# Kernel tuning notes

Measured on AMD Instinct MI355X. Metric: run time of the kernel, lower is better.

The kernel has to match this reference:

```python
import jax, jax.numpy as jnp
import numpy as np

N, H, K = 50000, 32, 15
C_IN, C_OUT = 64, 128
KP_EXTENT = 1.0
BN_EPS = 1e-5
SLOPE = 0.2


def setup_inputs() -> dict:
    key = jax.random.key(0)
    k1, k2, k3, k4, k5 = jax.random.split(key, 5)
    points = jax.random.normal(k1, (N, 3), dtype=jnp.float32)
    x = jax.random.normal(k2, (N, C_IN), dtype=jnp.float32)
    neighbors = jax.random.randint(k3, (N, H), 0, N, dtype=jnp.int32)
    # kernel points: fixed disposition inside the kernel sphere
    kernel_points = jax.random.normal(k4, (K, 3), dtype=jnp.float32) * (0.5 * KP_EXTENT)
    weights = jax.random.normal(k5, (K, C_IN, C_OUT), dtype=jnp.float32) / np.sqrt(K * C_IN)
    gamma = jnp.ones((C_OUT,), dtype=jnp.float32)
    beta = jnp.zeros((C_OUT,), dtype=jnp.float32)
    return {"points": points, "x": x, "neighbors": neighbors,
            "kernel_points": kernel_points, "weights": weights,
            "gamma": gamma, "beta": beta}


def reference(points, x, neighbors, kernel_points, weights, gamma, beta):
    # --- KPConv: irregular neighbor gather + kernel-point weighted sum ---
    # relative neighbor positions: [N, H, 3]
    neighb_pos = points[neighbors] - points[:, None, :]
    # squared distances to each kernel point: [N, H, K]
    sq_dist = jnp.sum((neighb_pos[:, :, None, :] - kernel_points[None, None, :, :]) ** 2, axis=-1)
    # linear correlation (influence), clipped at 0: [N, H, K]
    influence = jnp.maximum(0.0, 1.0 - jnp.sqrt(sq_dist) / KP_EXTENT)
    # gathered neighbor features: [N, H, C_in]
    neighb_x = x[neighbors]
    # per-kernel-point aggregated features: [N, K, C_in]
    weighted_feat = jnp.einsum('nhk,nhc->nkc', influence, neighb_x)
    # apply per-kernel-point weight matrices and sum: [N, C_out]
    out = jnp.einsum('nkc,kcd->nd', weighted_feat, weights)
    # --- BatchNorm1d (training-mode batch statistics) ---
    mean = jnp.mean(out, axis=0)
    var = jnp.var(out, axis=0)
    y = (out - mean) * jax.lax.rsqrt(var + BN_EPS) * gamma + beta
    # --- LeakyReLU(0.2) ---
    return jnp.where(y > 0, y, SLOPE * y)
```

## Files before the change

kernel.cpp:

```cpp
#include <hip/hip_runtime.h>
#include <hip/hip_bf16.h>

#define N_PTS 50000
#define H_NB 32
#define K_KP 15
#define C_IN 64
#define C_OUT 128
#define KC 960
#define M_PAD 50048
#define M_TILE 32
#define PPW 8
#define WFS 968
#define XG_SUB 68
#define XG_PLANE 552
#define XG_WAVE (4*XG_PLANE)
#define BN_EPS 1e-5f
#define SLOPE 0.2f

typedef __attribute__((ext_vector_type(8))) __bf16 bf16x8;
typedef __attribute__((ext_vector_type(8))) unsigned short ushort8;
typedef __attribute__((ext_vector_type(4))) float f32x4;

__device__ __forceinline__ unsigned short bfbits(float f){
  return __builtin_bit_cast(unsigned short, (__bf16)f);
}
__device__ __forceinline__ bf16x8 ld_bf8(const unsigned short* p){
  return __builtin_bit_cast(bf16x8, *(const uint4*)p);
}
__device__ __forceinline__ void gload16(const void* g, void* l){
  __builtin_amdgcn_global_load_lds(
      (__attribute__((address_space(1))) void*)(g),
      (__attribute__((address_space(3))) void*)(l), 16, 0, 0);
}

__global__ __launch_bounds__(256) void xprep_kernel(const float* __restrict__ x,
                                                    unsigned short* __restrict__ xbf){
  int t = blockIdx.x*blockDim.x + threadIdx.x;
  if (t < N_PTS*C_IN/8) {
    float4 a = ((const float4*)x)[2*t], b = ((const float4*)x)[2*t+1];
    ushort8 o;
    o[0]=bfbits(a.x); o[1]=bfbits(a.y); o[2]=bfbits(a.z); o[3]=bfbits(a.w);
    o[4]=bfbits(b.x); o[5]=bfbits(b.y); o[6]=bfbits(b.z); o[7]=bfbits(b.w);
    *(ushort8*)(xbf + 8*t) = o;
  }
}

__global__ __launch_bounds__(256) void prep_kernel(const float* __restrict__ W,
                                                   unsigned short* __restrict__ Wt,
                                                   float* __restrict__ stats){
  __shared__ float tile[32][33];
  if (blockIdx.x == 0 && blockIdx.y == 0 && threadIdx.x < 2*C_OUT)
    stats[threadIdx.x] = 0.f;
  const int kc0 = blockIdx.x * 32, d0 = blockIdx.y * 32;
  const int r = threadIdx.x >> 5, c = threadIdx.x & 31;
  #pragma unroll
  for (int rr = 0; rr < 4; ++rr) {
    int row = rr*8 + r;
    tile[row][c] = W[(size_t)(kc0+row)*C_OUT + d0 + c];
  }
  __syncthreads();
  #pragma unroll
  for (int rr = 0; rr < 4; ++rr) {
    int dr = rr*8 + r;
    Wt[(size_t)(d0+dr)*KC + kc0 + c] = bfbits(tile[c][dr]);
  }
}

template<bool SPLIT>
__global__ __launch_bounds__(256, SPLIT ? 4 : 2) void kpconv_core(
    const float* __restrict__ points,
    const float* __restrict__ x,
    const unsigned short* __restrict__ xbf,
    const int*   __restrict__ neighbors,
    const float* __restrict__ kpts,
    const unsigned short* __restrict__ Wt,
    unsigned short* __restrict__ wfg,
    float* __restrict__ out_pre,
    float* __restrict__ stats)
{
  __shared__ __align__(16) unsigned short xg[4 * XG_WAVE];
  __shared__ unsigned short wf_lds[SPLIT ? 8 : M_TILE*WFS];
  __shared__ float sh_sum[SPLIT ? 1 : C_OUT];
  __shared__ float sh_sq [SPLIT ? 1 : C_OUT];

  const int tid  = threadIdx.x;
  const int w    = tid >> 6;
  const int lane = tid & 63;
  const int l15  = lane & 15;
  const int lq   = lane >> 4;
  const int base = blockIdx.x * M_TILE;

  float kqx, kqy, kqz;
  if (l15 < K_KP) { kqx = kpts[l15*3+0]; kqy = kpts[l15*3+1]; kqz = kpts[l15*3+2]; }
  else            { kqx = 1e3f; kqy = 0.f; kqz = 0.f; }

  unsigned short* xgw = &xg[w * XG_WAVE];

  if constexpr (SPLIT) {
    int   idx_c, idx_n = 0, idx_nn = 0;
    float pcx, pcy, pcz, pnx = 0, pny = 0, pnz = 0;
    float ccx, ccy, ccz, cnx = 0, cny = 0, cnz = 0, c2x = 0, c2y = 0, c2z = 0;
    uint2 xr[8];
    {
      int n0 = base + w*PPW;  int nc0 = n0 < N_PTS ? n0 : N_PTS-1;
      idx_c = neighbors[nc0*H_NB + (lane & 31)];
      ccx = points[nc0*3+0]; ccy = points[nc0*3+1]; ccz = points[nc0*3+2];
      const float* pp = points + (size_t)idx_c*3;
      pcx = pp[0]; pcy = pp[1]; pcz = pp[2];
      #pragma unroll
      for (int it = 0; it < 8; ++it) {
        int nh = __shfl(idx_c, 4*it + lq);
        xr[it] = *(const uint2*)&xbf[(size_t)nh*C_IN + 4*l15];
      }
      int n1 = n0 + 1;  int nc1 = n1 < N_PTS ? n1 : N_PTS-1;
      idx_n = neighbors[nc1*H_NB + (lane & 31)];
      cnx = points[nc1*3+0]; cny = points[nc1*3+1]; cnz = points[nc1*3+2];
      const float* pq = points + (size_t)idx_n*3;
      pnx = pq[0]; pny = pq[1]; pnz = pq[2];
    }

    #pragma unroll 1
    for (int p = 0; p < PPW; ++p) {
      float rx = pcx - ccx, ry = pcy - ccy, rz = pcz - ccz;
      bf16x8 afrag;
      #pragma unroll
      for (int j = 0; j < 8; ++j) {
        int h = (lq << 3) + j;
        float dx = __shfl(rx, h) - kqx;
        float dy = __shfl(ry, h) - kqy;
        float dz = __shfl(rz, h) - kqz;
        float f  = 1.f - sqrtf(dx*dx + dy*dy + dz*dz);
        afrag[j] = (__bf16)(f > 0.f ? f : 0.f);
      }

      #pragma unroll
      for (int it = 0; it < 8; ++it) {
        int ei = XG_PLANE*(l15 >> 2) + XG_SUB*it + 16*lq + 4*(l15 & 3);
        *(uint2*)(xgw + ei) = xr[it];
      }

      if (p + 1 < PPW) {
        #pragma unroll
        for (int it = 0; it < 8; ++it) {
          int nh = __shfl(idx_n, 4*it + lq);
          xr[it] = *(const uint2*)&xbf[(size_t)nh*C_IN + 4*l15];
        }
      }
      if (p + 2 < PPW) {
        int n2 = base + w*PPW + p + 2;  int nc2 = n2 < N_PTS ? n2 : N_PTS-1;
        idx_nn = neighbors[nc2*H_NB + (lane & 31)];
        c2x = points[nc2*3+0]; c2y = points[nc2*3+1]; c2z = points[nc2*3+2];
      }

      asm volatile("s_waitcnt lgkmcnt(0)" ::: "memory");

      ushort8 bbr[4];
      #pragma unroll
      for (int ct = 0; ct < 4; ++ct) {
        #pragma unroll
        for (int j = 0; j < 8; ++j)
          bbr[ct][j] = xgw[XG_PLANE*ct + XG_SUB*(2*lq + (j>>2)) + 16*(j&3) + l15];
      }

      f32x4 acc[4] = {{0,0,0,0},{0,0,0,0},{0,0,0,0},{0,0,0,0}};
      #pragma unroll
      for (int ct = 0; ct < 4; ++ct)
        acc[ct] = __builtin_amdgcn_mfma_f32_16x16x32_bf16(
            afrag, __builtin_bit_cast(bf16x8, bbr[ct]), acc[ct], 0, 0, 0);

      const int n_out = base + w*PPW + p;
      #pragma unroll
      for (int ct = 0; ct < 4; ++ct) {
        #pragma unroll
        for (int r = 0; r < 4; ++r) {
          int k = 4*lq + r;
          if (k < K_KP)
            xgw[72*k + ct*16 + l15] = bfbits(acc[ct][r]);
        }
      }
      asm volatile("s_waitcnt lgkmcnt(0)" ::: "memory");
      if (n_out < N_PTS) {
        uint4 c0 = *(const uint4*)(xgw + 72*(lane>>3) + 8*(lane&7));
        *(uint4*)(wfg + (size_t)n_out*KC + lane*8) = c0;
        if (lane < 56) {
          int ch = 64 + lane;
          uint4 c1 = *(const uint4*)(xgw + 72*(ch>>3) + 8*(ch&7));
          *(uint4*)(wfg + (size_t)n_out*KC + ch*8) = c1;
        }
      }
      asm volatile("s_waitcnt lgkmcnt(0)" ::: "memory");

      if (p + 1 < PPW) {
        pcx = pnx; pcy = pny; pcz = pnz;
        ccx = cnx; ccy = cny; ccz = cnz;
        idx_c = idx_n; idx_n = idx_nn;
        cnx = c2x; cny = c2y; cnz = c2z;
        if (p + 2 < PPW) {
          const float* pq = points + (size_t)idx_n*3;
          pnx = pq[0]; pny = pq[1]; pnz = pq[2];
        }
      }
    }
  } else {
    {
      int   idx_c, idx_n = 0, idx_nn = 0;
      float pcx, pcy, pcz, pnx = 0, pny = 0, pnz = 0;
      float ccx, ccy, ccz, cnx = 0, cny = 0, cnz = 0, c2x = 0, c2y = 0, c2z = 0;
      float4 xr[8];
      {
        int n0 = base + w*PPW;  int nc0 = n0 < N_PTS ? n0 : N_PTS-1;
        idx_c = neighbors[nc0*H_NB + (lane & 31)];
        ccx = points[nc0*3+0]; ccy = points[nc0*3+1]; ccz = points[nc0*3+2];
        const float* pp = points + (size_t)idx_c*3;
        pcx = pp[0]; pcy = pp[1]; pcz = pp[2];
        #pragma unroll
        for (int it = 0; it < 8; ++it) {
          int nh = __shfl(idx_c, 4*it + lq);
          xr[it] = *(const float4*)&x[(size_t)nh*C_IN + 4*l15];
        }
        int n1 = n0 + 1;  int nc1 = n1 < N_PTS ? n1 : N_PTS-1;
        idx_n = neighbors[nc1*H_NB + (lane & 31)];
        cnx = points[nc1*3+0]; cny = points[nc1*3+1]; cnz = points[nc1*3+2];
        const float* pq = points + (size_t)idx_n*3;
        pnx = pq[0]; pny = pq[1]; pnz = pq[2];
      }

      #pragma unroll 1
      for (int p = 0; p < PPW; ++p) {
        const int mpt = w*PPW + p;
        float rx = pcx - ccx, ry = pcy - ccy, rz = pcz - ccz;
        bf16x8 afrag;
        #pragma unroll
        for (int j = 0; j < 8; ++j) {
          int h = (lq << 3) + j;
          float dx = __shfl(rx, h) - kqx;
          float dy = __shfl(ry, h) - kqy;
          float dz = __shfl(rz, h) - kqz;
          float f  = 1.f - sqrtf(dx*dx + dy*dy + dz*dz);
          afrag[j] = (__bf16)(f > 0.f ? f : 0.f);
        }
        #pragma unroll
        for (int it = 0; it < 8; ++it) {
          float4 v = xr[it];
          unsigned lo = ((unsigned)bfbits(v.y) << 16) | bfbits(v.x);
          unsigned hi = ((unsigned)bfbits(v.w) << 16) | bfbits(v.z);
          int ei = XG_PLANE*(l15 >> 2) + XG_SUB*it + 16*lq + 4*(l15 & 3);
          uint2 val; val.x = lo; val.y = hi;
          *(uint2*)(xgw + ei) = val;
        }
        if (p + 1 < PPW) {
          #pragma unroll
          for (int it = 0; it < 8; ++it) {
            int nh = __shfl(idx_n, 4*it + lq);
            xr[it] = *(const float4*)&x[(size_t)nh*C_IN + 4*l15];
          }
        }
        if (p + 2 < PPW) {
          int n2 = base + w*PPW + p + 2;  int nc2 = n2 < N_PTS ? n2 : N_PTS-1;
          idx_nn = neighbors[nc2*H_NB + (lane & 31)];
          c2x = points[nc2*3+0]; c2y = points[nc2*3+1]; c2z = points[nc2*3+2];
        }
        asm volatile("s_waitcnt lgkmcnt(0)" ::: "memory");
        ushort8 bbr[4];
        #pragma unroll
        for (int ct = 0; ct < 4; ++ct) {
          #pragma unroll
          for (int j = 0; j < 8; ++j)
            bbr[ct][j] = xgw[XG_PLANE*ct + XG_SUB*(2*lq + (j>>2)) + 16*(j&3) + l15];
        }
        f32x4 acc[4] = {{0,0,0,0},{0,0,0,0},{0,0,0,0},{0,0,0,0}};
        #pragma unroll
        for (int ct = 0; ct < 4; ++ct)
          acc[ct] = __builtin_amdgcn_mfma_f32_16x16x32_bf16(
              afrag, __builtin_bit_cast(bf16x8, bbr[ct]), acc[ct], 0, 0, 0);
        #pragma unroll
        for (int ct = 0; ct < 4; ++ct) {
          #pragma unroll
          for (int r = 0; r < 4; ++r) {
            int k = 4*lq + r;
            if (k < K_KP)
              wf_lds[mpt*WFS + k*C_IN + ((ct ^ lq)*16) + l15] = bfbits(acc[ct][r]);
          }
        }
        if (p + 1 < PPW) {
          pcx = pnx; pcy = pny; pcz = pnz;
          ccx = cnx; ccy = cny; ccz = cnz;
          idx_c = idx_n; idx_n = idx_nn;
          cnx = c2x; cny = c2y; cnz = c2z;
          if (p + 2 < PPW) {
            const float* pq = points + (size_t)idx_n*3;
            pnx = pq[0]; pny = pq[1]; pnz = pq[2];
          }
        }
      }
    }

    __syncthreads();
    const int wd = w;
    f32x4 b00{0,0,0,0}, b01{0,0,0,0}, b10{0,0,0,0}, b11{0,0,0,0};
    const unsigned short* arow0 = &wf_lds[l15*WFS];
    const unsigned short* arow1 = arow0 + 16*WFS;
    const unsigned short* wrow0 = Wt + (size_t)(wd*32 + l15)*KC + lq*8;
    const unsigned short* wrow1 = wrow0 + (size_t)16*KC;
    #pragma unroll 6
    for (int ks = 0; ks < KC/32; ++ks) {
      int aoff = (ks*32 + lq*8) ^ ((((ks >> 1) >> 2) & 3) << 4);
      bf16x8 a0 = ld_bf8(arow0 + aoff);
      bf16x8 a1 = ld_bf8(arow1 + aoff);
      bf16x8 w0 = ld_bf8(wrow0 + ks*32);
      bf16x8 w1 = ld_bf8(wrow1 + ks*32);
      b00 = __builtin_amdgcn_mfma_f32_16x16x32_bf16(a0, w0, b00, 0, 0, 0);
      b01 = __builtin_amdgcn_mfma_f32_16x16x32_bf16(a0, w1, b01, 0, 0, 0);
      b10 = __builtin_amdgcn_mfma_f32_16x16x32_bf16(a1, w0, b10, 0, 0, 0);
      b11 = __builtin_amdgcn_mfma_f32_16x16x32_bf16(a1, w1, b11, 0, 0, 0);
    }
    float s0 = 0.f, q0 = 0.f, s1 = 0.f, q1 = 0.f;
    const int dcol0 = wd*32 + l15;
    #pragma unroll
    for (int mi = 0; mi < 2; ++mi) {
      const f32x4 A0 = mi ? b10 : b00;
      const f32x4 A1 = mi ? b11 : b01;
      #pragma unroll
      for (int r = 0; r < 4; ++r) {
        int n = base + mi*16 + 4*lq + r;
        if (n < N_PTS) {
          float v0 = A0[r], v1 = A1[r];
          out_pre[(size_t)n*C_OUT + dcol0]      = v0;
          out_pre[(size_t)n*C_OUT + dcol0 + 16] = v1;
          s0 += v0; q0 += v0*v0;
          s1 += v1; q1 += v1*v1;
        }
      }
    }
    s0 += __shfl_xor(s0, 16); s0 += __shfl_xor(s0, 32);
    q0 += __shfl_xor(q0, 16); q0 += __shfl_xor(q0, 32);
    s1 += __shfl_xor(s1, 16); s1 += __shfl_xor(s1, 32);
    q1 += __shfl_xor(q1, 16); q1 += __shfl_xor(q1, 32);
    if (lane < 16) {
      sh_sum[wd*32 + lane]      = s0;
      sh_sum[wd*32 + 16 + lane] = s1;
      sh_sq [wd*32 + lane]      = q0;
      sh_sq [wd*32 + 16 + lane] = q1;
    }
    __syncthreads();
    if (tid < C_OUT) {
      atomicAdd(&stats[tid],         sh_sum[tid]);
      atomicAdd(&stats[C_OUT + tid], sh_sq[tid]);
    }
  }
}

__global__ __launch_bounds__(256, 2) void gemm_kernel(
    const unsigned short* __restrict__ wfg,
    const unsigned short* __restrict__ Wt,
    float* __restrict__ out_pre,
    float* __restrict__ stats)
{
  __shared__ __align__(16) unsigned short Abuf[3][64*64];
  __shared__ __align__(16) unsigned short Bbuf[3][128*64];
  __shared__ float sh_sum[2][C_OUT];
  __shared__ float sh_sq [2][C_OUT];

  const int tid  = threadIdx.x;
  const int w    = tid >> 6;
  const int lane = tid & 63;
  const int l15  = lane & 15;
  const int lq   = lane >> 4;
  const int wm   = w >> 1;
  const int wn   = w & 1;
  const int m0   = blockIdx.x * 64;

  const int r8 = lane >> 3;
  const int cs = (lane & 7) ^ r8;

  auto stage = [&](int b, int kt){
    const int k0 = kt * 64;
    #pragma unroll
    for (int q = 0; q < 2; ++q) {
      int row = w*16 + q*8;
      gload16(wfg + (size_t)(m0 + row + r8)*KC + k0 + cs*8, &Abuf[b][row*64]);
    }
    #pragma unroll
    for (int q = 0; q < 4; ++q) {
      int row = w*32 + q*8;
      gload16(Wt + (size_t)(row + r8)*KC + k0 + cs*8, &Bbuf[b][row*64]);
    }
  };

  stage(0, 0);
  stage(1, 1);

  f32x4 acc[2][4] = {};
  const int NT = KC / 64;
  for (int ks = 0; ks < NT; ++ks) {
    if (ks + 1 < NT) {
      asm volatile("s_waitcnt vmcnt(6)" ::: "memory");
    } else {
      asm volatile("s_waitcnt vmcnt(0)" ::: "memory");
    }
    __builtin_amdgcn_sched_barrier(0);
    __builtin_amdgcn_s_barrier();
    asm volatile("" ::: "memory");
    if (ks + 2 < NT) stage((ks + 2) % 3, ks + 2);

    const unsigned short* A = Abuf[ks % 3];
    const unsigned short* B = Bbuf[ks % 3];
    #pragma unroll
    for (int kk = 0; kk < 2; ++kk) {
      const int cA = kk*4 + lq;
      bf16x8 af[2], bfr[4];
      #pragma unroll
      for (int mf = 0; mf < 2; ++mf) {
        int r = wm*32 + mf*16 + l15;
        af[mf] = ld_bf8(A + r*64 + ((cA ^ (r & 7)) * 8));
      }
      #pragma unroll
      for (int nf = 0; nf < 4; ++nf) {
        int r = wn*64 + nf*16 + l15;
        bfr[nf] = ld_bf8(B + r*64 + ((cA ^ (r & 7)) * 8));
      }
      #pragma unroll
      for (int mf = 0; mf < 2; ++mf)
        #pragma unroll
        for (int nf = 0; nf < 4; ++nf)
          acc[mf][nf] = __builtin_amdgcn_mfma_f32_16x16x32_bf16(af[mf], bfr[nf], acc[mf][nf], 0, 0, 0);
    }
  }

  float ssum[4] = {0,0,0,0}, ssq[4] = {0,0,0,0};
  #pragma unroll
  for (int mf = 0; mf < 2; ++mf) {
    #pragma unroll
    for (int nf = 0; nf < 4; ++nf) {
      #pragma unroll
      for (int r = 0; r < 4; ++r) {
        int m = m0 + wm*32 + mf*16 + 4*lq + r;
        if (m < N_PTS) {
          float v = acc[mf][nf][r];
          out_pre[(size_t)m*C_OUT + wn*64 + nf*16 + l15] = v;
          ssum[nf] += v; ssq[nf] += v*v;
        }
      }
    }
  }
  #pragma unroll
  for (int nf = 0; nf < 4; ++nf) {
    ssum[nf] += __shfl_xor(ssum[nf], 16); ssum[nf] += __shfl_xor(ssum[nf], 32);
    ssq[nf]  += __shfl_xor(ssq[nf], 16);  ssq[nf]  += __shfl_xor(ssq[nf], 32);
  }
  if (lane < 16) {
    #pragma unroll
    for (int nf = 0; nf < 4; ++nf) {
      sh_sum[wm][wn*64 + nf*16 + lane] = ssum[nf];
      sh_sq [wm][wn*64 + nf*16 + lane] = ssq[nf];
    }
  }
  __syncthreads();
  if (tid < C_OUT) {
    atomicAdd(&stats[tid],         sh_sum[0][tid] + sh_sum[1][tid]);
    atomicAdd(&stats[C_OUT + tid], sh_sq[0][tid] + sh_sq[1][tid]);
  }
}

__global__ __launch_bounds__(256) void bn_lrelu_kernel(float* __restrict__ out,
                                                       const float* __restrict__ stats,
                                                       const float* __restrict__ gamma,
                                                       const float* __restrict__ beta){
  __shared__ float sc_s[C_OUT], sh_s[C_OUT];
  if (threadIdx.x < C_OUT) {
    int d = threadIdx.x;
    float mean = stats[d] * (1.f/N_PTS);
    float var  = stats[C_OUT+d] * (1.f/N_PTS) - mean*mean;
    var = var > 0.f ? var : 0.f;
    float inv = rsqrtf(var + BN_EPS);
    float sc  = inv * gamma[d];
    sc_s[d] = sc;
    sh_s[d] = beta[d] - mean * sc;
  }
  __syncthreads();
  const int total4 = N_PTS*C_OUT/4;
  const float4* scp = (const float4*)sc_s;
  const float4* shp = (const float4*)sh_s;
  float4* o4 = (float4*)out;
  for (int t = blockIdx.x*blockDim.x + threadIdx.x; t < total4; t += gridDim.x*blockDim.x) {
    int col4 = t & (C_OUT/4 - 1);
    float4 v = o4[t];
    float4 sc = scp[col4], sh = shp[col4];
    float y0 = v.x*sc.x + sh.x;
    float y1 = v.y*sc.y + sh.y;
    float y2 = v.z*sc.z + sh.z;
    float y3 = v.w*sc.w + sh.w;
    v.x = y0 > 0.f ? y0 : SLOPE*y0;
    v.y = y1 > 0.f ? y1 : SLOPE*y1;
    v.z = y2 > 0.f ? y2 : SLOPE*y2;
    v.w = y3 > 0.f ? y3 : SLOPE*y3;
    o4[t] = v;
  }
}

extern "C" void kernel_launch(void* const* d_in, const int* in_sizes, int n_in,
                              void* d_out, int out_size, void* d_ws, size_t ws_size,
                              hipStream_t stream) {
  const float* points    = (const float*)d_in[0];
  const float* x         = (const float*)d_in[1];
  const int*   neighbors = (const int*)d_in[2];
  const float* kpts      = (const float*)d_in[3];
  const float* weights   = (const float*)d_in[4];
  const float* gamma     = (const float*)d_in[5];
  const float* beta      = (const float*)d_in[6];
  float* out = (float*)d_out;
  float* ws  = (float*)d_ws;
  unsigned short* Wt  = (unsigned short*)((char*)d_ws + 2048);
  unsigned short* wfg = (unsigned short*)((char*)d_ws + 2048 + 245760);
  unsigned short* xbf = (unsigned short*)d_out;
  const size_t need = 2048u + 245760u + (size_t)M_PAD*KC*2u;
  const bool split = (ws_size >= need);

  hipLaunchKernelGGL(prep_kernel, dim3(KC/32, C_OUT/32), dim3(256), 0, stream,
                     weights, Wt, ws);
  const int nblocks = (N_PTS + M_TILE - 1) / M_TILE;
  if (split) {
    hipLaunchKernelGGL(xprep_kernel, dim3((N_PTS*C_IN/8 + 255)/256), dim3(256), 0, stream,
                       x, xbf);
    kpconv_core<true><<<dim3(nblocks), dim3(256), 0, stream>>>(
        points, x, xbf, neighbors, kpts, Wt, wfg, out, ws);
    gemm_kernel<<<dim3(M_PAD/64), dim3(256), 0, stream>>>(wfg, Wt, out, ws);
  } else {
    kpconv_core<false><<<dim3(nblocks), dim3(256), 0, stream>>>(
        points, x, xbf, neighbors, kpts, Wt, wfg, out, ws);
  }
  hipLaunchKernelGGL(bn_lrelu_kernel, dim3(2048), dim3(256), 0, stream, out, ws, gamma, beta);
}
```

Before: 120.2 us.

## Gather neighbor features directly into double-buffered LDS with swizzled layout

In the split KPConv path, neighbor bf16 feature rows are now loaded straight from global memory into LDS with a direct-to-LDS load helper, instead of being staged through registers and then written to LDS. Two per-wave LDS buffers alternate, so the gather for the next point overlaps the MFMA and output work for the current one, and explicit vmcnt waits control when data is ready. An XOR swizzle on column chunks is meant to avoid bank conflicts when reading the B operand. This raises LDS use per block and depends on vmcnt counting that other outstanding global operations can disturb.

```diff
diff --git a/kernel.cpp b/kernel.cpp
--- a/kernel.cpp
+++ b/kernel.cpp
@@ -78,7 +78,7 @@
     float* __restrict__ out_pre,
     float* __restrict__ stats)
 {
-  __shared__ __align__(16) unsigned short xg[4 * XG_WAVE];
+  __shared__ __align__(16) unsigned short xg[SPLIT ? 4*4096 : 4*XG_WAVE];
   __shared__ unsigned short wf_lds[SPLIT ? 8 : M_TILE*WFS];
   __shared__ float sh_sum[SPLIT ? 1 : C_OUT];
   __shared__ float sh_sq [SPLIT ? 1 : C_OUT];
@@ -94,30 +94,42 @@
   if (l15 < K_KP) { kqx = kpts[l15*3+0]; kqy = kpts[l15*3+1]; kqz = kpts[l15*3+2]; }
   else            { kqx = 1e3f; kqy = 0.f; kqz = 0.f; }
 
-  unsigned short* xgw = &xg[w * XG_WAVE];
-
   if constexpr (SPLIT) {
+    unsigned short* xb0 = &xg[w * 4096];
+    unsigned short* xb1 = xb0 + 2048;
+
+    const int r8 = lane >> 3;
+    const int pc = lane & 7;
+
+    auto dma_point = [&](unsigned short* buf, int idx){
+      #pragma unroll
+      for (int it = 0; it < 4; ++it) {
+        int nh = __shfl(idx, 8*it + r8);
+        const unsigned short* src = xbf + (size_t)nh*C_IN + ((pc ^ (2*it)) * 8);
+        gload16(src, buf + it*512);
+      }
+    };
+
     int   idx_c, idx_n = 0, idx_nn = 0;
     float pcx, pcy, pcz, pnx = 0, pny = 0, pnz = 0;
     float ccx, ccy, ccz, cnx = 0, cny = 0, cnz = 0, c2x = 0, c2y = 0, c2z = 0;
-    uint2 xr[8];
     {
       int n0 = base + w*PPW;  int nc0 = n0 < N_PTS ? n0 : N_PTS-1;
       idx_c = neighbors[nc0*H_NB + (lane & 31)];
       ccx = points[nc0*3+0]; ccy = points[nc0*3+1]; ccz = points[nc0*3+2];
       const float* pp = points + (size_t)idx_c*3;
       pcx = pp[0]; pcy = pp[1]; pcz = pp[2];
-      #pragma unroll
-      for (int it = 0; it < 8; ++it) {
-        int nh = __shfl(idx_c, 4*it + lq);
-        xr[it] = *(const uint2*)&xbf[(size_t)nh*C_IN + 4*l15];
-      }
       int n1 = n0 + 1;  int nc1 = n1 < N_PTS ? n1 : N_PTS-1;
       idx_n = neighbors[nc1*H_NB + (lane & 31)];
       cnx = points[nc1*3+0]; cny = points[nc1*3+1]; cnz = points[nc1*3+2];
       const float* pq = points + (size_t)idx_n*3;
       pnx = pq[0]; pny = pq[1]; pnz = pq[2];
-    }
+      dma_point(xb0, idx_c);
+      dma_point(xb1, idx_n);
+    }
+
+    unsigned short* cur = xb0;
+    unsigned short* nxt = xb1;
 
     #pragma unroll 1
     for (int p = 0; p < PPW; ++p) {
@@ -133,40 +145,27 @@
         afrag[j] = (__bf16)(f > 0.f ? f : 0.f);
       }
 
-      #pragma unroll
-      for (int it = 0; it < 8; ++it) {
-        int ei = XG_PLANE*(l15 >> 2) + XG_SUB*it + 16*lq + 4*(l15 & 3);
-        *(uint2*)(xgw + ei) = xr[it];
-      }
-
-      if (p + 1 < PPW) {
-        #pragma unroll
-        for (int it = 0; it < 8; ++it) {
-          int nh = __shfl(idx_n, 4*it + lq);
-          xr[it] = *(const uint2*)&xbf[(size_t)nh*C_IN + 4*l15];
-        }
-      }
       if (p + 2 < PPW) {
         int n2 = base + w*PPW + p + 2;  int nc2 = n2 < N_PTS ? n2 : N_PTS-1;
         idx_nn = neighbors[nc2*H_NB + (lane & 31)];
         c2x = points[nc2*3+0]; c2y = points[nc2*3+1]; c2z = points[nc2*3+2];
       }
 
-      asm volatile("s_waitcnt lgkmcnt(0)" ::: "memory");
-
-      ushort8 bbr[4];
+      if (p + 1 < PPW) { asm volatile("s_waitcnt vmcnt(4)" ::: "memory"); }
+      else             { asm volatile("s_waitcnt vmcnt(0)" ::: "memory"); }
+      __builtin_amdgcn_sched_barrier(0);
+
+      f32x4 acc[4] = {{0,0,0,0},{0,0,0,0},{0,0,0,0},{0,0,0,0}};
       #pragma unroll
       for (int ct = 0; ct < 4; ++ct) {
+        ushort8 b;
+        const int pcr = ((2*ct + (l15 >> 3)) ^ (2*lq)) * 8 + (l15 & 7);
         #pragma unroll
         for (int j = 0; j < 8; ++j)
-          bbr[ct][j] = xgw[XG_PLANE*ct + XG_SUB*(2*lq + (j>>2)) + 16*(j&3) + l15];
-      }
-
-      f32x4 acc[4] = {{0,0,0,0},{0,0,0,0},{0,0,0,0},{0,0,0,0}};
-      #pragma unroll
-      for (int ct = 0; ct < 4; ++ct)
+          b[j] = cur[lq*512 + j*64 + pcr];
         acc[ct] = __builtin_amdgcn_mfma_f32_16x16x32_bf16(
-            afrag, __builtin_bit_cast(bf16x8, bbr[ct]), acc[ct], 0, 0, 0);
+            afrag, __builtin_bit_cast(bf16x8, b), acc[ct], 0, 0, 0);
+      }
 
       const int n_out = base + w*PPW + p;
       #pragma unroll
@@ -175,16 +174,16 @@
         for (int r = 0; r < 4; ++r) {
           int k = 4*lq + r;
           if (k < K_KP)
-            xgw[72*k + ct*16 + l15] = bfbits(acc[ct][r]);
+            cur[72*k + ct*16 + l15] = bfbits(acc[ct][r]);
         }
       }
       asm volatile("s_waitcnt lgkmcnt(0)" ::: "memory");
       if (n_out < N_PTS) {
-        uint4 c0 = *(const uint4*)(xgw + 72*(lane>>3) + 8*(lane&7));
+        uint4 c0 = *(const uint4*)(cur + 72*(lane>>3) + 8*(lane&7));
         *(uint4*)(wfg + (size_t)n_out*KC + lane*8) = c0;
         if (lane < 56) {
           int ch = 64 + lane;
-          uint4 c1 = *(const uint4*)(xgw + 72*(ch>>3) + 8*(ch&7));
+          uint4 c1 = *(const uint4*)(cur + 72*(ch>>3) + 8*(ch&7));
           *(uint4*)(wfg + (size_t)n_out*KC + ch*8) = c1;
         }
       }
@@ -198,10 +197,13 @@
         if (p + 2 < PPW) {
           const float* pq = points + (size_t)idx_n*3;
           pnx = pq[0]; pny = pq[1]; pnz = pq[2];
-        }
+          dma_point(cur, idx_n);
+        }
+        unsigned short* t = cur; cur = nxt; nxt = t;
       }
     }
   } else {
+    unsigned short* xgw = &xg[w * XG_WAVE];
     {
       int   idx_c, idx_n = 0, idx_nn = 0;
       float pcx, pcy, pcz, pnx = 0, pny = 0, pnz = 0;
```

Result: faster. 116.1 us, median of 2 (-3.4%).

## Merge x/W prep kernels and deepen gather pipeline with swizzled LDS layout

Applied to the files above, without the earlier changes.

Folds the bf16 conversion of x into the weight-transpose prep kernel so one launch does both. The split-path core kernel now double-buffers neighbour feature gathers two points ahead, using 16-byte loads. It stores them in a smaller XOR-swizzled per-wave LDS buffer, which cuts LDS per block and raises the occupancy target from 4 to 5 blocks. The aim is to hide gather latency and reduce launch overhead, at the cost of more registers held live across iterations. The non-split path now also runs the x conversion, which writes into the output buffer and is wasted work there.

```diff
diff --git a/kernel.cpp b/kernel.cpp
--- a/kernel.cpp
+++ b/kernel.cpp
@@ -14,6 +14,7 @@
 #define XG_SUB 68
 #define XG_PLANE 552
 #define XG_WAVE (4*XG_PLANE)
+#define XPB ((N_PTS*C_IN/8 + 255)/256)
 #define BN_EPS 1e-5f
 #define SLOPE 0.2f
 
@@ -33,25 +34,28 @@
       (__attribute__((address_space(3))) void*)(l), 16, 0, 0);
 }
 
-__global__ __launch_bounds__(256) void xprep_kernel(const float* __restrict__ x,
-                                                    unsigned short* __restrict__ xbf){
-  int t = blockIdx.x*blockDim.x + threadIdx.x;
-  if (t < N_PTS*C_IN/8) {
-    float4 a = ((const float4*)x)[2*t], b = ((const float4*)x)[2*t+1];
-    ushort8 o;
-    o[0]=bfbits(a.x); o[1]=bfbits(a.y); o[2]=bfbits(a.z); o[3]=bfbits(a.w);
-    o[4]=bfbits(b.x); o[5]=bfbits(b.y); o[6]=bfbits(b.z); o[7]=bfbits(b.w);
-    *(ushort8*)(xbf + 8*t) = o;
-  }
-}
-
 __global__ __launch_bounds__(256) void prep_kernel(const float* __restrict__ W,
+                                                   const float* __restrict__ x,
                                                    unsigned short* __restrict__ Wt,
+                                                   unsigned short* __restrict__ xbf,
                                                    float* __restrict__ stats){
   __shared__ float tile[32][33];
-  if (blockIdx.x == 0 && blockIdx.y == 0 && threadIdx.x < 2*C_OUT)
+  int b = blockIdx.x;
+  if (b < XPB) {
+    int t = b*256 + threadIdx.x;
+    if (t < N_PTS*C_IN/8) {
+      float4 a = ((const float4*)x)[2*t], v = ((const float4*)x)[2*t+1];
+      ushort8 o;
+      o[0]=bfbits(a.x); o[1]=bfbits(a.y); o[2]=bfbits(a.z); o[3]=bfbits(a.w);
+      o[4]=bfbits(v.x); o[5]=bfbits(v.y); o[6]=bfbits(v.z); o[7]=bfbits(v.w);
+      *(ushort8*)(xbf + 8*t) = o;
+    }
+    return;
+  }
+  b -= XPB;
+  const int kc0 = (b % (KC/32)) * 32, d0 = (b / (KC/32)) * 32;
+  if (kc0 == 0 && d0 == 0 && threadIdx.x < 2*C_OUT)
     stats[threadIdx.x] = 0.f;
-  const int kc0 = blockIdx.x * 32, d0 = blockIdx.y * 32;
   const int r = threadIdx.x >> 5, c = threadIdx.x & 31;
   #pragma unroll
   for (int rr = 0; rr < 4; ++rr) {
@@ -67,7 +71,7 @@
 }
 
 template<bool SPLIT>
-__global__ __launch_bounds__(256, SPLIT ? 4 : 2) void kpconv_core(
+__global__ __launch_bounds__(256, SPLIT ? 5 : 2) void kpconv_core(
     const float* __restrict__ points,
     const float* __restrict__ x,
     const unsigned short* __restrict__ xbf,
@@ -78,7 +82,7 @@
     float* __restrict__ out_pre,
     float* __restrict__ stats)
 {
-  __shared__ __align__(16) unsigned short xg[4 * XG_WAVE];
+  __shared__ __align__(16) unsigned short xg[SPLIT ? 4*2048 : 4*XG_WAVE];
   __shared__ unsigned short wf_lds[SPLIT ? 8 : M_TILE*WFS];
   __shared__ float sh_sum[SPLIT ? 1 : C_OUT];
   __shared__ float sh_sq [SPLIT ? 1 : C_OUT];
@@ -94,34 +98,78 @@
   if (l15 < K_KP) { kqx = kpts[l15*3+0]; kqy = kpts[l15*3+1]; kqz = kpts[l15*3+2]; }
   else            { kqx = 1e3f; kqy = 0.f; kqz = 0.f; }
 
-  unsigned short* xgw = &xg[w * XG_WAVE];
-
   if constexpr (SPLIT) {
-    int   idx_c, idx_n = 0, idx_nn = 0;
-    float pcx, pcy, pcz, pnx = 0, pny = 0, pnz = 0;
-    float ccx, ccy, ccz, cnx = 0, cny = 0, cnz = 0, c2x = 0, c2y = 0, c2z = 0;
-    uint2 xr[8];
+    unsigned short* xbuf = &xg[w * 2048];
+    const int r8 = lane >> 3;
+    const int pc = lane & 7;
+
+    int   idx0, idx1 = 0, idx2 = 0, idx3 = 0;
+    float c0x, c0y, c0z, c1x = 0, c1y = 0, c1z = 0;
+    float c2x = 0, c2y = 0, c2z = 0, c3x = 0, c3y = 0, c3z = 0;
+    float p0x, p0y, p0z, p1x = 0, p1y = 0, p1z = 0;
+    uint4 xrA[4], xrB[4];
+
     {
-      int n0 = base + w*PPW;  int nc0 = n0 < N_PTS ? n0 : N_PTS-1;
-      idx_c = neighbors[nc0*H_NB + (lane & 31)];
-      ccx = points[nc0*3+0]; ccy = points[nc0*3+1]; ccz = points[nc0*3+2];
-      const float* pp = points + (size_t)idx_c*3;
-      pcx = pp[0]; pcy = pp[1]; pcz = pp[2];
-      #pragma unroll
-      for (int it = 0; it < 8; ++it) {
-        int nh = __shfl(idx_c, 4*it + lq);
-        xr[it] = *(const uint2*)&xbf[(size_t)nh*C_IN + 4*l15];
-      }
-      int n1 = n0 + 1;  int nc1 = n1 < N_PTS ? n1 : N_PTS-1;
-      idx_n = neighbors[nc1*H_NB + (lane & 31)];
-      cnx = points[nc1*3+0]; cny = points[nc1*3+1]; cnz = points[nc1*3+2];
-      const float* pq = points + (size_t)idx_n*3;
-      pnx = pq[0]; pny = pq[1]; pnz = pq[2];
-    }
-
-    #pragma unroll 1
+      int n0 = base + w*PPW;
+      int nc0 = n0 < N_PTS ? n0 : N_PTS-1;
+      idx0 = neighbors[nc0*H_NB + (lane & 31)];
+      c0x = points[nc0*3+0]; c0y = points[nc0*3+1]; c0z = points[nc0*3+2];
+      const float* pp = points + (size_t)idx0*3;
+      p0x = pp[0]; p0y = pp[1]; p0z = pp[2];
+      int nc1 = (n0+1) < N_PTS ? (n0+1) : N_PTS-1;
+      idx1 = neighbors[nc1*H_NB + (lane & 31)];
+      c1x = points[nc1*3+0]; c1y = points[nc1*3+1]; c1z = points[nc1*3+2];
+      const float* pq = points + (size_t)idx1*3;
+      p1x = pq[0]; p1y = pq[1]; p1z = pq[2];
+      int nc2 = (n0+2) < N_PTS ? (n0+2) : N_PTS-1;
+      idx2 = neighbors[nc2*H_NB + (lane & 31)];
+      c2x = points[nc2*3+0]; c2y = points[nc2*3+1]; c2z = points[nc2*3+2];
+      #pragma unroll
+      for (int it = 0; it < 4; ++it) {
+        int nh = __shfl(idx0, 8*it + r8);
+        xrA[it] = *(const uint4*)(xbf + (size_t)nh*C_IN + ((pc ^ (2*it)) * 8));
+      }
+      #pragma unroll
+      for (int it = 0; it < 4; ++it) {
+        int nh = __shfl(idx1, 8*it + r8);
+        xrB[it] = *(const uint4*)(xbf + (size_t)nh*C_IN + ((pc ^ (2*it)) * 8));
+      }
+    }
+
+    #pragma unroll 2
     for (int p = 0; p < PPW; ++p) {
-      float rx = pcx - ccx, ry = pcy - ccy, rz = pcz - ccz;
+      if ((p & 1) == 0) {
+        #pragma unroll
+        for (int it = 0; it < 4; ++it)
+          *(uint4*)(xbuf + it*512 + lane*8) = xrA[it];
+        if (p + 2 < PPW) {
+          #pragma unroll
+          for (int it = 0; it < 4; ++it) {
+            int nh = __shfl(idx2, 8*it + r8);
+            xrA[it] = *(const uint4*)(xbf + (size_t)nh*C_IN + ((pc ^ (2*it)) * 8));
+          }
+        }
+      } else {
+        #pragma unroll
+        for (int it = 0; it < 4; ++it)
+          *(uint4*)(xbuf + it*512 + lane*8) = xrB[it];
+        if (p + 2 < PPW) {
+          #pragma unroll
+          for (int it = 0; it < 4; ++it) {
+            int nh = __shfl(idx2, 8*it + r8);
+            xrB[it] = *(const uint4*)(xbf + (size_t)nh*C_IN + ((pc ^ (2*it)) * 8));
+          }
+        }
+      }
+
+      if (p + 3 < PPW) {
+        int n3 = base + w*PPW + p + 3;
+        int nc3 = n3 < N_PTS ? n3 : N_PTS-1;
+        idx3 = neighbors[nc3*H_NB + (lane & 31)];
+        c3x = points[nc3*3+0]; c3y = points[nc3*3+1]; c3z = points[nc3*3+2];
+      }
+
+      float rx = p0x - c0x, ry = p0y - c0y, rz = p0z - c0z;
       bf16x8 afrag;
       #pragma unroll
       for (int j = 0; j < 8; ++j) {
@@ -133,40 +181,20 @@
         afrag[j] = (__bf16)(f > 0.f ? f : 0.f);
       }
 
-      #pragma unroll
-      for (int it = 0; it < 8; ++it) {
-        int ei = XG_PLANE*(l15 >> 2) + XG_SUB*it + 16*lq + 4*(l15 & 3);
-        *(uint2*)(xgw + ei) = xr[it];
-      }
-
-      if (p + 1 < PPW) {
-        #pragma unroll
-        for (int it = 0; it < 8; ++it) {
-          int nh = __shfl(idx_n, 4*it + lq);
-          xr[it] = *(const uint2*)&xbf[(size_t)nh*C_IN + 4*l15];
-        }
-      }
-      if (p + 2 < PPW) {
-        int n2 = base + w*PPW + p + 2;  int nc2 = n2 < N_PTS ? n2 : N_PTS-1;
-        idx_nn = neighbors[nc2*H_NB + (lane & 31)];
-        c2x = points[nc2*3+0]; c2y = points[nc2*3+1]; c2z = points[nc2*3+2];
-      }
-
       asm volatile("s_waitcnt lgkmcnt(0)" ::: "memory");
-
-      ushort8 bbr[4];
+      __builtin_amdgcn_sched_barrier(0);
+
+      f32x4 acc[4] = {{0,0,0,0},{0,0,0,0},{0,0,0,0},{0,0,0,0}};
       #pragma unroll
       for (int ct = 0; ct < 4; ++ct) {
+        ushort8 bb;
+        const int pcr = ((2*ct + (l15 >> 3)) ^ (2*lq)) * 8 + (l15 & 7);
         #pragma unroll
         for (int j = 0; j < 8; ++j)
-          bbr[ct][j] = xgw[XG_PLANE*ct + XG_SUB*(2*lq + (j>>2)) + 16*(j&3) + l15];
-      }
-
-      f32x4 acc[4] = {{0,0,0,0},{0,0,0,0},{0,0,0,0},{0,0,0,0}};
-      #pragma unroll
-      for (int ct = 0; ct < 4; ++ct)
+          bb[j] = xbuf[lq*512 + j*64 + pcr];
         acc[ct] = __builtin_amdgcn_mfma_f32_16x16x32_bf16(
-            afrag, __builtin_bit_cast(bf16x8, bbr[ct]), acc[ct], 0, 0, 0);
+            afrag, __builtin_bit_cast(bf16x8, bb), acc[ct], 0, 0, 0);
+      }
 
       const int n_out = base + w*PPW + p;
       #pragma unroll
@@ -175,33 +203,33 @@
         for (int r = 0; r < 4; ++r) {
           int k = 4*lq + r;
           if (k < K_KP)
-            xgw[72*k + ct*16 + l15] = bfbits(acc[ct][r]);
+            xbuf[72*k + ct*16 + l15] = bfbits(acc[ct][r]);
         }
       }
       asm volatile("s_waitcnt lgkmcnt(0)" ::: "memory");
       if (n_out < N_PTS) {
-        uint4 c0 = *(const uint4*)(xgw + 72*(lane>>3) + 8*(lane&7));
-        *(uint4*)(wfg + (size_t)n_out*KC + lane*8) = c0;
+        uint4 s0 = *(const uint4*)(xbuf + 72*(lane>>3) + 8*(lane&7));
+        *(uint4*)(wfg + (size_t)n_out*KC + lane*8) = s0;
         if (lane < 56) {
           int ch = 64 + lane;
-          uint4 c1 = *(const uint4*)(xgw + 72*(ch>>3) + 8*(ch&7));
-          *(uint4*)(wfg + (size_t)n_out*KC + ch*8) = c1;
+          uint4 s1 = *(const uint4*)(xbuf + 72*(ch>>3) + 8*(ch&7));
+          *(uint4*)(wfg + (size_t)n_out*KC + ch*8) = s1;
         }
       }
       asm volatile("s_waitcnt lgkmcnt(0)" ::: "memory");
 
-      if (p + 1 < PPW) {
-        pcx = pnx; pcy = pny; pcz = pnz;
-        ccx = cnx; ccy = cny; ccz = cnz;
-        idx_c = idx_n; idx_n = idx_nn;
-        cnx = c2x; cny = c2y; cnz = c2z;
-        if (p + 2 < PPW) {
-          const float* pq = points + (size_t)idx_n*3;
-          pnx = pq[0]; pny = pq[1]; pnz = pq[2];
-        }
+      idx0 = idx1; idx1 = idx2; idx2 = idx3;
+      c0x = c1x; c0y = c1y; c0z = c1z;
+      c1x = c2x; c1y = c2y; c1z = c2z;
+      c2x = c3x; c2y = c3y; c2z = c3z;
+      p0x = p1x; p0y = p1y; p0z = p1z;
+      if (p + 2 < PPW) {
+        const float* pq = points + (size_t)idx1*3;
+        p1x = pq[0]; p1y = pq[1]; p1z = pq[2];
       }
     }
   } else {
+    unsigned short* xgw = &xg[w * XG_WAVE];
     {
       int   idx_c, idx_n = 0, idx_nn = 0;
       float pcx, pcy, pcz, pnx = 0, pny = 0, pnz = 0;
@@ -516,16 +544,16 @@
   const size_t need = 2048u + 245760u + (size_t)M_PAD*KC*2u;
   const bool split = (ws_size >= need);
 
-  hipLaunchKernelGGL(prep_kernel, dim3(KC/32, C_OUT/32), dim3(256), 0, stream,
-                     weights, Wt, ws);
   const int nblocks = (N_PTS + M_TILE - 1) / M_TILE;
   if (split) {
-    hipLaunchKernelGGL(xprep_kernel, dim3((N_PTS*C_IN/8 + 255)/256), dim3(256), 0, stream,
-                       x, xbf);
+    hipLaunchKernelGGL(prep_kernel, dim3(XPB + (KC/32)*(C_OUT/32)), dim3(256), 0, stream,
+                       weights, x, Wt, xbf, ws);
     kpconv_core<true><<<dim3(nblocks), dim3(256), 0, stream>>>(
         points, x, xbf, neighbors, kpts, Wt, wfg, out, ws);
     gemm_kernel<<<dim3(M_PAD/64), dim3(256), 0, stream>>>(wfg, Wt, out, ws);
   } else {
+    hipLaunchKernelGGL(prep_kernel, dim3(XPB + (KC/32)*(C_OUT/32)), dim3(256), 0, stream,
+                       weights, x, Wt, xbf, ws);
     kpconv_core<false><<<dim3(nblocks), dim3(256), 0, stream>>>(
         points, x, xbf, neighbors, kpts, Wt, wfg, out, ws);
   }
```

Result: slower. 173.4 us (+44.3%).
